# Kernel optimization log

Measured on AMD Instinct MI355X. Metric: run time of the kernel, lower is better.

Reference implementation:

```python
import jax, jax.numpy as jnp
import numpy as np

N = 1_000_000   # num nodes
D = 128         # embedding dimension (order=1, no halving)
T = 100         # number of SGD batches (all with alpha = init_alpha, i.e. b < 100)
B = 1024        # batch_size
K = 6           # 1 positive + negative=5 samples per edge
ALPHA = 0.025   # init_alpha


def setup_inputs() -> dict:
    key = jax.random.key(0)
    k1, k2, k3 = jax.random.split(key, 3)
    # original init: (np.random.random((N, D)) - 0.5) / D
    emb_vertex = (jax.random.uniform(k1, (N, D), dtype=jnp.float32) - 0.5) / D
    u_idx = jax.random.randint(k2, (T, B), 0, N)          # sampled edge sources
    tgt_idx = jax.random.randint(k3, (T, B, K), 0, N)     # col 0: positive v, cols 1..5: negatives
    return {"emb_vertex": emb_vertex, "u_idx": u_idx, "tgt_idx": tgt_idx}


def reference(emb_vertex, u_idx, tgt_idx):
    # labels: positive (j=0) -> 1, negatives -> 0
    label = jnp.zeros((B, K), emb_vertex.dtype).at[:, 0].set(1.0)

    def step(emb, batch):
        u, tgt = batch                                    # [B], [B, K]
        vec_u = emb[u]                                    # [B, D] (numpy fancy-index copy)
        vec_v = emb[tgt]                                  # [B, K, D]
        f = jax.nn.sigmoid(jnp.einsum('bd,bkd->bk', vec_u, vec_v))  # [B, K]
        g = ALPHA * (label - f)                           # [B, K]
        # vec_error accumulated over the 1+negative inner iterations
        vec_error = jnp.einsum('bk,bkd->bd', g, vec_v)    # [B, D]
        # so only emb_vertex[u] += vec_error persists.
        emb = emb.at[u].add(vec_error)
        return emb, None

    emb_final, _ = jax.lax.scan(step, emb_vertex, (u_idx, tgt_idx))
    # final L2 row-normalization (sklearn preprocessing.normalize(emb, 'l2'))
    norm = jnp.maximum(jnp.linalg.norm(emb_final, axis=1, keepdims=True), 1e-12)
    return emb_final / norm
```

## Files before the change

### kernel.cpp

```cpp
#include <hip/hip_runtime.h>

typedef unsigned int uint;

#define N_NODES 1000000
#define D       128
#define T_STEPS 100
#define B       1024
#define K       6
#define ALPHA   0.025f

#define CNBLK  1280
#define CTPB   256
#define CHUNK  10
#define NCHUNK (T_STEPS / CHUNK)
#define CE     (CHUNK * B)
#define NWAVES (CNBLK * CTPB / 64)
#define EPW    (CE / NWAVES)

#define RPC     20
#define SLICE_A 12
#define SLICE_B 8

#define FLAG_OFF     65536
#define CNT_BYTES    ((size_t)FLAG_OFF * 4)
#define SPARSE_BYTES ((size_t)(FLAG_OFF + N_NODES) * 4)

__device__ __forceinline__ float wave_sum(float v) {
#pragma unroll
    for (int off = 32; off; off >>= 1) v += __shfl_xor(v, off, 64);
    return v;
}

__device__ __forceinline__ uint aloadu(const uint* p) {
    return __hip_atomic_load(p, __ATOMIC_RELAXED, __HIP_MEMORY_SCOPE_AGENT);
}

__device__ __forceinline__ void norm_slice(const float* __restrict__ emb_in,
                                           float* __restrict__ out,
                                           const uint* __restrict__ flags,
                                           int lane, int r0, int nrows)
{
    for (int j0 = 0; j0 < nrows; j0 += 4) {
        float2 v[4];
        int    act[4];
#pragma unroll
        for (int j = 0; j < 4; ++j) {
            const int r = r0 + j0 + j;
            act[j] = (r < N_NODES) && (flags[r] == 0u);
            if (act[j])
                v[j] = *(const float2*)(emb_in + (size_t)r * D + 2 * lane);
        }
#pragma unroll
        for (int j = 0; j < 4; ++j) {
            if (act[j]) {
                const float ss  = wave_sum(v[j].x * v[j].x + v[j].y * v[j].y);
                const float inv = 1.f / fmaxf(sqrtf(ss), 1e-12f);
                const int r = r0 + j0 + j;
                *(float2*)(out + (size_t)r * D + 2 * lane) =
                    make_float2(v[j].x * inv, v[j].y * inv);
            }
        }
    }
}

__device__ __forceinline__ void bar_arrive(uint* ws_u, int k) {
    __syncthreads();
    if (threadIdx.x == 0)
        atomicAdd(&ws_u[k * 2048 + (int)blockIdx.x], 1u);
}
__device__ __forceinline__ void bar_wait_acq(uint* ws_u, int k) {
    __syncthreads();
    if (threadIdx.x < 64) {
        const uint* s = ws_u + k * 2048 + threadIdx.x;
        for (;;) {
            int got = 0;
#pragma unroll
            for (int i = 0; i < CNBLK / 64; ++i) got += (aloadu(s + i * 64) != 0u);
            if (got == CNBLK / 64) break;
        }
    }
    __syncthreads();
    if (threadIdx.x == 0)
        __builtin_amdgcn_fence(__ATOMIC_ACQUIRE, "agent");
    __syncthreads();
}

template <bool SPARSE>
__global__ __launch_bounds__(256) void prologue(const float* __restrict__ emb_in,
                                                const int*   __restrict__ u_idx,
                                                float*       __restrict__ out,
                                                uint*        __restrict__ flags)
{
    if (SPARSE) {
        const int wave = (blockIdx.x * 256 + threadIdx.x) >> 6;
        const int lane = threadIdx.x & 63;
        const int nw = gridDim.x * 4;
        for (int e = wave; e < T_STEPS * B; e += nw) {
            const int r = u_idx[e];
            if (lane == 0) flags[r] = 1u;
            const size_t off = (size_t)r * D + 2 * lane;
            *(float2*)(out + off) = *(const float2*)(emb_in + off);
        }
    } else {
        const int tid = blockIdx.x * 256 + threadIdx.x;
        const int stride = gridDim.x * 256;
        const float4* src = (const float4*)emb_in;
        float4*       dst = (float4*)out;
        for (int i = tid; i < N_NODES * D / 4; i += stride) dst[i] = src[i];
    }
}

template <bool SPARSE>
__global__ __launch_bounds__(CTPB) void line_loop(const float* __restrict__ emb_in,
                                                  const int*   __restrict__ u_idx,
                                                  const int*   __restrict__ tgt_idx,
                                                  float*       __restrict__ out,
                                                  uint*        ws_u)
{
    const int w    = (blockIdx.x * CTPB + threadIdx.x) >> 6;
    const int lane = threadIdx.x & 63;
    const uint* flags = ws_u + FLAG_OFF;

    for (int c = 0; c < NCHUNK; ++c) {
        int    cu[EPW];
        float2 e2[EPW];
        {
            float2 u2l[EPW];
            float2 v2l[EPW][K];
#pragma unroll
            for (int jj = 0; jj < EPW; ++jj) {
                const int e = c * CE + w + jj * NWAVES;
                const int u = u_idx[e];
                cu[jj] = u;
                u2l[jj] = *(const float2*)(out + (size_t)u * D + 2 * lane);
#pragma unroll
                for (int k = 0; k < K; ++k) {
                    const int v = tgt_idx[e * K + k];
                    const float* src = (SPARSE && !flags[v]) ? emb_in : out;
                    v2l[jj][k] = *(const float2*)(src + (size_t)v * D + 2 * lane);
                }
            }

            if (SPARSE)
                norm_slice(emb_in, out, flags, lane,
                           (c * NWAVES + w) * RPC, SLICE_A);

#pragma unroll
            for (int jj = 0; jj < EPW; ++jj) {
                float2 acc = make_float2(0.f, 0.f);
#pragma unroll
                for (int k = 0; k < K; ++k) {
                    const float s = wave_sum(u2l[jj].x * v2l[jj][k].x +
                                             u2l[jj].y * v2l[jj][k].y);
                    const float f = 1.f / (1.f + __expf(-s));
                    const float gg = ALPHA * ((k == 0 ? 1.f : 0.f) - f);
                    acc.x += gg * v2l[jj][k].x;
                    acc.y += gg * v2l[jj][k].y;
                }
                e2[jj] = acc;
            }
        }

#pragma unroll
        for (int jj = 0; jj < EPW; ++jj) {
            float* urow = out + (size_t)cu[jj] * D + 2 * lane;
            atomicAdd(urow,     e2[jj].x);
            atomicAdd(urow + 1, e2[jj].y);
        }

        bar_arrive(ws_u, c);

        if (SPARSE)
            norm_slice(emb_in, out, flags, lane,
                       (c * NWAVES + w) * RPC + SLICE_A, SLICE_B);

        if (c + 1 < NCHUNK)
            bar_wait_acq(ws_u, c);
    }
}

__global__ __launch_bounds__(256) void normalize_flagged(float* __restrict__ out,
                                                         const uint* __restrict__ flags)
{
    const int wave = (blockIdx.x * 256 + threadIdx.x) >> 6;
    const int lane = threadIdx.x & 63;
    const int nw = gridDim.x * 4;
    for (int r0 = wave * 4; r0 < N_NODES; r0 += nw * 4) {
        const uint4 f4 = *(const uint4*)(flags + r0);
        if (!(f4.x | f4.y | f4.z | f4.w)) continue;
        const uint fl[4] = { f4.x, f4.y, f4.z, f4.w };
#pragma unroll
        for (int j = 0; j < 4; ++j) {
            if (fl[j]) {
                float2* p = (float2*)(out + (size_t)(r0 + j) * D + 2 * lane);
                const float2 v = *p;
                const float ss  = wave_sum(v.x * v.x + v.y * v.y);
                const float inv = 1.f / fmaxf(sqrtf(ss), 1e-12f);
                *p = make_float2(v.x * inv, v.y * inv);
            }
        }
    }
}

__global__ __launch_bounds__(256) void normalize_all(float* __restrict__ out)
{
    const int wave = (blockIdx.x * 256 + threadIdx.x) >> 6;
    const int lane = threadIdx.x & 63;
    const int nw = gridDim.x * 4;
    for (int r0 = wave * 4; r0 < N_NODES; r0 += nw * 4) {
#pragma unroll
        for (int j = 0; j < 4; ++j) {
            float2* p = (float2*)(out + (size_t)(r0 + j) * D + 2 * lane);
            const float2 v = *p;
            const float ss  = wave_sum(v.x * v.x + v.y * v.y);
            const float inv = 1.f / fmaxf(sqrtf(ss), 1e-12f);
            *p = make_float2(v.x * inv, v.y * inv);
        }
    }
}

extern "C" void kernel_launch(void* const* d_in, const int* in_sizes, int n_in,
                              void* d_out, int out_size, void* d_ws, size_t ws_size,
                              hipStream_t stream)
{
    const float* emb_in  = (const float*)d_in[0];
    const int*   u_idx   = (const int*)d_in[1];
    const int*   tgt_idx = (const int*)d_in[2];
    float*       out     = (float*)d_out;
    uint*        ws_u    = (uint*)d_ws;
    uint*        flags   = ws_u + FLAG_OFF;

    const bool sparse = ws_size >= SPARSE_BYTES;
    hipMemsetAsync(d_ws, 0, sparse ? SPARSE_BYTES : CNT_BYTES, stream);

    if (sparse) {
        prologue<true>  <<<1024, 256, 0, stream>>>(emb_in, u_idx, out, flags);
        line_loop<true> <<<CNBLK, CTPB, 0, stream>>>(emb_in, u_idx, tgt_idx, out, ws_u);
        normalize_flagged<<<2048, 256, 0, stream>>>(out, flags);
    } else {
        prologue<false>  <<<2048, 256, 0, stream>>>(emb_in, u_idx, out, flags);
        line_loop<false> <<<CNBLK, CTPB, 0, stream>>>(emb_in, u_idx, tgt_idx, out, ws_u);
        normalize_all<<<2048, 256, 0, stream>>>(out);
    }
}
```

Baseline: 544.1 us.

## Split untouched-row normalization into dedicated blocks running beside SGD blocks

Normalization of rows that SGD never touches moves out of the SGD waves, which used to interleave it around the grid barrier. It now runs in 768 separate blocks launched in the same grid as the 1280 SGD blocks. The SGD blocks keep only the gather, update and barrier, and the barrier arrive and wait are merged into one call. The intent is to overlap the bandwidth-heavy normalization with the latency-bound SGD chunks. The risk is that all 2048 blocks must be co-resident for the spin barrier, and the extra blocks compete with the SGD blocks for CU resources.

```diff
diff --git a/kernel.cpp b/kernel.cpp
--- a/kernel.cpp
+++ b/kernel.cpp
@@ -9,17 +9,16 @@
 #define K       6
 #define ALPHA   0.025f
 
-#define CNBLK  1280
+#define SGDB   1280
+#define NORMB  768
+#define TOTB   (SGDB + NORMB)
 #define CTPB   256
 #define CHUNK  10
 #define NCHUNK (T_STEPS / CHUNK)
 #define CE     (CHUNK * B)
-#define NWAVES (CNBLK * CTPB / 64)
+#define NWAVES (SGDB * CTPB / 64)
 #define EPW    (CE / NWAVES)
-
-#define RPC     20
-#define SLICE_A 12
-#define SLICE_B 8
+#define NNW    (NORMB * CTPB / 64)
 
 #define FLAG_OFF     65536
 #define CNT_BYTES    ((size_t)FLAG_OFF * 4)
@@ -35,48 +34,17 @@
     return __hip_atomic_load(p, __ATOMIC_RELAXED, __HIP_MEMORY_SCOPE_AGENT);
 }
 
-__device__ __forceinline__ void norm_slice(const float* __restrict__ emb_in,
-                                           float* __restrict__ out,
-                                           const uint* __restrict__ flags,
-                                           int lane, int r0, int nrows)
-{
-    for (int j0 = 0; j0 < nrows; j0 += 4) {
-        float2 v[4];
-        int    act[4];
-#pragma unroll
-        for (int j = 0; j < 4; ++j) {
-            const int r = r0 + j0 + j;
-            act[j] = (r < N_NODES) && (flags[r] == 0u);
-            if (act[j])
-                v[j] = *(const float2*)(emb_in + (size_t)r * D + 2 * lane);
-        }
-#pragma unroll
-        for (int j = 0; j < 4; ++j) {
-            if (act[j]) {
-                const float ss  = wave_sum(v[j].x * v[j].x + v[j].y * v[j].y);
-                const float inv = 1.f / fmaxf(sqrtf(ss), 1e-12f);
-                const int r = r0 + j0 + j;
-                *(float2*)(out + (size_t)r * D + 2 * lane) =
-                    make_float2(v[j].x * inv, v[j].y * inv);
-            }
-        }
-    }
-}
-
-__device__ __forceinline__ void bar_arrive(uint* ws_u, int k) {
+__device__ __forceinline__ void bar_sync_acq(uint* ws_u, int k) {
     __syncthreads();
     if (threadIdx.x == 0)
         atomicAdd(&ws_u[k * 2048 + (int)blockIdx.x], 1u);
-}
-__device__ __forceinline__ void bar_wait_acq(uint* ws_u, int k) {
-    __syncthreads();
     if (threadIdx.x < 64) {
         const uint* s = ws_u + k * 2048 + threadIdx.x;
         for (;;) {
             int got = 0;
 #pragma unroll
-            for (int i = 0; i < CNBLK / 64; ++i) got += (aloadu(s + i * 64) != 0u);
-            if (got == CNBLK / 64) break;
+            for (int i = 0; i < SGDB / 64; ++i) got += (aloadu(s + i * 64) != 0u);
+            if (got == SGDB / 64) break;
         }
     }
     __syncthreads();
@@ -111,15 +79,46 @@
 }
 
 template <bool SPARSE>
-__global__ __launch_bounds__(CTPB) void line_loop(const float* __restrict__ emb_in,
-                                                  const int*   __restrict__ u_idx,
-                                                  const int*   __restrict__ tgt_idx,
-                                                  float*       __restrict__ out,
-                                                  uint*        ws_u)
-{
-    const int w    = (blockIdx.x * CTPB + threadIdx.x) >> 6;
+__global__ __launch_bounds__(CTPB, 8) void fused(const float* __restrict__ emb_in,
+                                                 const int*   __restrict__ u_idx,
+                                                 const int*   __restrict__ tgt_idx,
+                                                 float*       __restrict__ out,
+                                                 uint*        ws_u)
+{
     const int lane = threadIdx.x & 63;
     const uint* flags = ws_u + FLAG_OFF;
+
+    if ((int)blockIdx.x >= SGDB) {
+        if (!SPARSE) return;
+        const int nwv = (((int)blockIdx.x - SGDB) * CTPB + (int)threadIdx.x) >> 6;
+        const int per = (N_NODES + NNW - 1) / NNW;
+        const int rb = nwv * per;
+        const int re = (rb + per < N_NODES) ? rb + per : N_NODES;
+        for (int r0 = rb; r0 < re; r0 += 8) {
+            float2 v[8];
+            uint   fl[8];
+#pragma unroll
+            for (int j = 0; j < 8; ++j) {
+                const int r = r0 + j;
+                const int ok = (r < re);
+                fl[j] = ok ? flags[r] : 1u;
+                v[j]  = ok ? *(const float2*)(emb_in + (size_t)r * D + 2 * lane)
+                           : make_float2(0.f, 0.f);
+            }
+#pragma unroll
+            for (int j = 0; j < 8; ++j) {
+                if (fl[j] == 0u) {
+                    const float ss  = wave_sum(v[j].x * v[j].x + v[j].y * v[j].y);
+                    const float inv = 1.f / fmaxf(sqrtf(ss), 1e-12f);
+                    *(float2*)(out + (size_t)(r0 + j) * D + 2 * lane) =
+                        make_float2(v[j].x * inv, v[j].y * inv);
+                }
+            }
+        }
+        return;
+    }
+
+    const int w = ((int)blockIdx.x * CTPB + (int)threadIdx.x) >> 6;
 
     for (int c = 0; c < NCHUNK; ++c) {
         int    cu[EPW];
@@ -140,11 +139,6 @@
                     v2l[jj][k] = *(const float2*)(src + (size_t)v * D + 2 * lane);
                 }
             }
-
-            if (SPARSE)
-                norm_slice(emb_in, out, flags, lane,
-                           (c * NWAVES + w) * RPC, SLICE_A);
-
 #pragma unroll
             for (int jj = 0; jj < EPW; ++jj) {
                 float2 acc = make_float2(0.f, 0.f);
@@ -168,14 +162,8 @@
             atomicAdd(urow + 1, e2[jj].y);
         }
 
-        bar_arrive(ws_u, c);
-
-        if (SPARSE)
-            norm_slice(emb_in, out, flags, lane,
-                       (c * NWAVES + w) * RPC + SLICE_A, SLICE_B);
-
         if (c + 1 < NCHUNK)
-            bar_wait_acq(ws_u, c);
+            bar_sync_acq(ws_u, c);
     }
 }
 
@@ -234,12 +222,12 @@
     hipMemsetAsync(d_ws, 0, sparse ? SPARSE_BYTES : CNT_BYTES, stream);
 
     if (sparse) {
-        prologue<true>  <<<1024, 256, 0, stream>>>(emb_in, u_idx, out, flags);
-        line_loop<true> <<<CNBLK, CTPB, 0, stream>>>(emb_in, u_idx, tgt_idx, out, ws_u);
+        prologue<true>   <<<1024, 256, 0, stream>>>(emb_in, u_idx, out, flags);
+        fused<true>      <<<TOTB, CTPB, 0, stream>>>(emb_in, u_idx, tgt_idx, out, ws_u);
         normalize_flagged<<<2048, 256, 0, stream>>>(out, flags);
     } else {
         prologue<false>  <<<2048, 256, 0, stream>>>(emb_in, u_idx, out, flags);
-        line_loop<false> <<<CNBLK, CTPB, 0, stream>>>(emb_in, u_idx, tgt_idx, out, ws_u);
-        normalize_all<<<2048, 256, 0, stream>>>(out);
-    }
-}
+        fused<false>     <<<TOTB, CTPB, 0, stream>>>(emb_in, u_idx, tgt_idx, out, ws_u);
+        normalize_all    <<<2048, 256, 0, stream>>>(out);
+    }
+}
```

Result: slower. 732.1 us (+34.5%).
